# Performance work log

Hardware: AMD Instinct MI355X
Metric: run time of the kernel (lower is better)

The kernel has to match this reference:

```python
import jax, jax.numpy as jnp
import numpy as np

N, E, H, S, F = 50000, 800000, 96, 48, 24


def _mlp(x, W1, b1, W2, b2):
    # equinox MLP depth=1: Linear -> relu -> Linear (identity final activation)
    h = jax.nn.relu(x @ W1.T + b1)
    return h @ W2.T + b2


def _segment_softmax(scores, seg, num_segments):
    mx = jax.ops.segment_max(scores, seg, num_segments=num_segments)
    e = jnp.exp(scores - mx[seg])
    s = jax.ops.segment_sum(e, seg, num_segments=num_segments)
    return e / (s[seg] + 1e-9)


def setup_inputs() -> dict:
    key = jax.random.key(0)
    ks = jax.random.split(key, 32)
    def p(i, shape):
        return jax.random.normal(ks[i], shape, dtype=jnp.float32) * 0.05
    in_attn = 2 * H + 2 * S + F   # 312
    w_attn = 2 * H                # 192
    gin = 3 * H                   # 288
    inp = {
        "x": p(0, (N, H)),
        "x_s": p(1, (N, S)),
        "edge_features": p(2, (E, F)),
        "edge_index": jax.random.randint(ks[3], (2, E), 0, N),
        # fwd attention MLP: in_attn -> w_attn -> 1
        "fwd_W1": p(4, (w_attn, in_attn)), "fwd_b1": p(5, (w_attn,)),
        "fwd_W2": p(6, (1, w_attn)), "fwd_b2": p(7, (1,)),
        # rev gate MLP: in_attn -> w_attn -> 1
        "rev_W1": p(8, (w_attn, in_attn)), "rev_b1": p(9, (w_attn,)),
        "rev_W2": p(10, (1, w_attn)), "rev_b2": p(11, (1,)),
        # reset gate MLP: 3H -> 3H -> H
        "reset_W1": p(12, (gin, gin)), "reset_b1": p(13, (gin,)),
        "reset_W2": p(14, (H, gin)), "reset_b2": p(15, (H,)),
        # update gate MLP: 3H -> 3H -> H
        "update_W1": p(16, (gin, gin)), "update_b1": p(17, (gin,)),
        "update_W2": p(18, (H, gin)), "update_b2": p(19, (H,)),
        # candidate MLP: 3H -> 3H -> H
        "cand_W1": p(20, (gin, gin)), "cand_b1": p(21, (gin,)),
        "cand_W2": p(22, (H, gin)), "cand_b2": p(23, (H,)),
    }
    return inp


def reference(x, x_s, edge_features, edge_index,
              fwd_W1, fwd_b1, fwd_W2, fwd_b2,
              rev_W1, rev_b1, rev_W2, rev_b2,
              reset_W1, reset_b1, reset_W2, reset_b2,
              update_W1, update_b1, update_W2, update_b2,
              cand_W1, cand_b1, cand_W2, cand_b2):
    num_nodes = x.shape[0]
    src, dest = edge_index[0], edge_index[1]

    def compute_messages(s, d, W1, b1, W2, b2, use_softmax):
        feat = jnp.concatenate([x[s], x[d], x_s[s], x_s[d], edge_features], axis=-1)
        raw = _mlp(feat, W1, b1, W2, b2)[:, 0]  # [E]
        if use_softmax:
            raw = jax.nn.leaky_relu(raw) / jnp.sqrt(jnp.asarray(x.shape[-1], dtype=x.dtype))
            w = _segment_softmax(raw, d, num_nodes)
        else:
            w = jax.nn.sigmoid(raw)
        agg = jax.ops.segment_sum(x[s] * w[:, None], d, num_segments=num_nodes)
        return agg, w

    fwd_msgs, fwd_w = compute_messages(src, dest, fwd_W1, fwd_b1, fwd_W2, fwd_b2, True)
    rev_msgs, rev_w = compute_messages(dest, src, rev_W1, rev_b1, rev_W2, rev_b2, False)

    messages = jnp.concatenate([fwd_msgs, rev_msgs], axis=-1)  # [N, 2H]
    gate_input = jnp.concatenate([x, messages], axis=-1)        # [N, 3H]
    r_gate = jax.nn.sigmoid(_mlp(gate_input, reset_W1, reset_b1, reset_W2, reset_b2))
    z_gate = jax.nn.sigmoid(_mlp(gate_input, update_W1, update_b1, update_W2, update_b2))
    cand_input = jnp.concatenate([r_gate * x, messages], axis=-1)
    candidate = jnp.tanh(_mlp(cand_input, cand_W1, cand_b1, cand_W2, cand_b2))
    update = (1 - z_gate) * x + z_gate * candidate
    return (update, fwd_w, rev_w, z_gate, r_gate)
```

## Files before the change

### kernel.cpp

```cpp
#include <hip/hip_runtime.h>
#include <math.h>

typedef unsigned short u16;
typedef unsigned int   u32;

#define HDIM 96
#define SDIM 48
#define FDIM 24
#define KA   312
#define WATT 192
#define KG   288

#define KT_A  10
#define KT_G  9
#define NS    296

#define NFRAG (2 * KT_A * 12 * 64)
#define W1F_Q (KT_G * 18 * 64)
#define W2F_Q (KT_G * 6 * 64)
#define NODEF_Q (3 * (W1F_Q + W2F_Q))

#define PB_EDGE 60
#define PB_W1   41
#define PB_W2   14
#define PB_NODE (3 * (PB_W1 + PB_W2))

typedef __attribute__((ext_vector_type(8))) __bf16 bf16x8;
typedef __attribute__((ext_vector_type(4))) float  f32x4;

__device__ __forceinline__ u16 f2bf(float f) {
  u32 u = __float_as_uint(f);
  u = (u + 0x7FFFu + ((u >> 16) & 1u)) >> 16;
  return (u16)u;
}
__device__ __forceinline__ float bf2f(u16 v) {
  return __uint_as_float((u32)v << 16);
}
__device__ __forceinline__ u32 pack2(float a, float b) {
  return (u32)f2bf(a) | ((u32)f2bf(b) << 16);
}
__device__ __forceinline__ f32x4 mfma_bf16(bf16x8 a, bf16x8 b, f32x4 c) {
  return __builtin_amdgcn_mfma_f32_16x16x32_bf16(a, b, c, 0, 0, 0);
}

__global__ __launch_bounds__(256) void prep_all(
    const float* __restrict__ fW1, const float* __restrict__ rW1,
    uint4* __restrict__ Bfrag,
    const float* __restrict__ W1r, const float* __restrict__ W2r,
    const float* __restrict__ W1u, const float* __restrict__ W2u,
    const float* __restrict__ W1c, const float* __restrict__ W2c,
    uint4* __restrict__ NodeF,
    const float* __restrict__ x, const float* __restrict__ xs,
    u32* __restrict__ xb, u32* __restrict__ xsb, int N)
{
  int b = blockIdx.x;
  const int tid = threadIdx.x;

  if (b < PB_EDGE) {
    const int idx = b * 256 + tid;
    const int lane = idx & 63;
    const int frag = idx >> 6;
    const int nt   = frag % 12;
    const int rest = frag / 12;
    const int kt   = rest % KT_A;
    const int mlp  = rest / KT_A;
    const int q = lane >> 4, c = lane & 15;
    const int n  = nt * 16 + c;
    const int p0 = kt * 16 + q * 4;
    const float* W = mlp ? rW1 : fW1;
    u32 v[4];
#pragma unroll
    for (int w = 0; w < 4; ++w) {
      const int p = p0 + w;
      u32 val = 0u;
      if (p < 156) {
        int src = p;
        if (mlp) {
          if (src < 48)       src += 48;
          else if (src < 96)  src -= 48;
          else if (src < 120) src += 24;
          else if (src < 144) src -= 24;
        }
        const float2 wv = *(const float2*)(W + (size_t)n * KA + 2 * src);
        val = pack2(wv.x, wv.y);
      }
      v[w] = val;
    }
    Bfrag[idx] = make_uint4(v[0], v[1], v[2], v[3]);
    return;
  }
  b -= PB_EDGE;

  if (b < PB_NODE) {
    const int mlp = b / (PB_W1 + PB_W2);
    const int lb  = b % (PB_W1 + PB_W2);
    const float* W;
    uint4* o;
    int NT, idx;
    if (lb < PB_W1) {
      NT = 18; idx = lb * 256 + tid;
      W = (mlp == 0) ? W1r : (mlp == 1) ? W1u : W1c;
      o = NodeF + (size_t)mlp * (W1F_Q + W2F_Q);
    } else {
      NT = 6; idx = (lb - PB_W1) * 256 + tid;
      W = (mlp == 0) ? W2r : (mlp == 1) ? W2u : W2c;
      o = NodeF + (size_t)mlp * (W1F_Q + W2F_Q) + W1F_Q;
    }
    if (idx >= KT_G * NT * 64) return;
    const int lane = idx & 63;
    const int frag = idx >> 6;
    const int nt = frag % NT, kt = frag / NT;
    const int q = lane >> 4, c = lane & 15;
    const int n = nt * 16 + c;
    const int k0 = kt * 32 + q * 8;
    u32 v[4];
#pragma unroll
    for (int w = 0; w < 4; ++w) {
      const float2 wv = *(const float2*)(W + (size_t)n * KG + k0 + 2 * w);
      v[w] = pack2(wv.x, wv.y);
    }
    o[idx] = make_uint4(v[0], v[1], v[2], v[3]);
    return;
  }
  b -= PB_NODE;

  {
    const int i = b * 256 + tid;
    const int nx = N * 48;
    if (i < nx) {
      const float2 v = ((const float2*)x)[i];
      xb[i] = pack2(v.x, v.y);
    } else if (i < nx + N * 24) {
      const float2 v = ((const float2*)xs)[i - nx];
      xsb[i - nx] = pack2(v.x, v.y);
    }
  }
}

__global__ __launch_bounds__(256, 2) void edge_kernel(
    const u32* __restrict__ xb, const u32* __restrict__ xsb,
    const float* __restrict__ ef, const int* __restrict__ ei,
    const u16* __restrict__ Bfrag,
    const float* __restrict__ fb1, const float* __restrict__ fW2,
    const float* __restrict__ fb2,
    const float* __restrict__ rb1, const float* __restrict__ rW2,
    const float* __restrict__ rb2,
    float* __restrict__ pe, float* __restrict__ out_revw, int N, int E)
{
  __shared__ float red[2][4][64];

  const int tid  = threadIdx.x;
  const int wave = tid >> 6, lane = tid & 63;
  const int q = lane >> 4, c = lane & 15;
  const int e0 = blockIdx.x * 64;

  int em[4], sm[4], dm[4];
#pragma unroll
  for (int m = 0; m < 4; ++m) {
    em[m] = min(e0 + m * 16 + c, E - 1);
    int s = ei[em[m]], d = ei[(size_t)E + em[m]];
    sm[m] = min(max(s, 0), N - 1);
    dm[m] = min(max(d, 0), N - 1);
  }

  const bf16x8* __restrict__ Bf = (const bf16x8*)Bfrag;

  f32x4 accF[4][3], accR[4][3];
#pragma unroll
  for (int m = 0; m < 4; ++m)
    for (int t = 0; t < 3; ++t) {
      accF[m][t] = (f32x4){0.f, 0.f, 0.f, 0.f};
      accR[m][t] = (f32x4){0.f, 0.f, 0.f, 0.f};
    }

#pragma unroll
  for (int kt = 0; kt < KT_A; ++kt) {
    const int p0 = kt * 16 + q * 4;
    bf16x8 a[4];
#pragma unroll
    for (int m = 0; m < 4; ++m) {
      uint4 av;
      if (kt < 3) {
        av = *(const uint4*)(xb + (size_t)sm[m] * 48 + p0);
      } else if (kt < 6) {
        av = *(const uint4*)(xb + (size_t)dm[m] * 48 + (p0 - 48));
      } else if (kt == 6) {
        av = *(const uint4*)(xsb + (size_t)sm[m] * 24 + (p0 - 96));
      } else if (kt == 7) {
        const u32* p = (q < 2) ? xsb + (size_t)sm[m] * 24 + (p0 - 96)
                               : xsb + (size_t)dm[m] * 24 + (p0 - 120);
        av = *(const uint4*)p;
      } else if (kt == 8) {
        av = *(const uint4*)(xsb + (size_t)dm[m] * 24 + (p0 - 120));
      } else {
        if (q < 3) {
          const float* efp = ef + (size_t)em[m] * 24 + (p0 - 144) * 2;
          const float4 f0 = *(const float4*)efp;
          const float4 f1 = *(const float4*)(efp + 4);
          av = make_uint4(pack2(f0.x, f0.y), pack2(f0.z, f0.w),
                          pack2(f1.x, f1.y), pack2(f1.z, f1.w));
        } else {
          av = make_uint4(0u, 0u, 0u, 0u);
        }
      }
      a[m] = __builtin_bit_cast(bf16x8, av);
    }
#pragma unroll
    for (int t = 0; t < 3; ++t) {
      const bf16x8 bF = Bf[((kt * 12) + wave * 3 + t) * 64 + lane];
      const bf16x8 bR = Bf[(((KT_A + kt) * 12) + wave * 3 + t) * 64 + lane];
#pragma unroll
      for (int m = 0; m < 4; ++m) {
        accF[m][t] = mfma_bf16(a[m], bF, accF[m][t]);
        accR[m][t] = mfma_bf16(a[m], bR, accR[m][t]);
      }
    }
  }

  float pf[4][4], pr[4][4];
#pragma unroll
  for (int m = 0; m < 4; ++m)
    for (int r = 0; r < 4; ++r) { pf[m][r] = 0.f; pr[m][r] = 0.f; }
#pragma unroll
  for (int t = 0; t < 3; ++t) {
    const int n = (wave * 3 + t) * 16 + c;
    const float fb = fb1[n], fw = fW2[n];
    const float rb = rb1[n], rw = rW2[n];
#pragma unroll
    for (int m = 0; m < 4; ++m)
      for (int r = 0; r < 4; ++r) {
        float hf = accF[m][t][r] + fb;
        hf = hf > 0.f ? hf : 0.f;
        pf[m][r] += hf * fw;
        float hr = accR[m][t][r] + rb;
        hr = hr > 0.f ? hr : 0.f;
        pr[m][r] += hr * rw;
      }
  }
  for (int off = 1; off <= 8; off <<= 1)
#pragma unroll
    for (int m = 0; m < 4; ++m)
      for (int r = 0; r < 4; ++r) {
        pf[m][r] += __shfl_xor(pf[m][r], off, 64);
        pr[m][r] += __shfl_xor(pr[m][r], off, 64);
      }

  if (c == 0) {
#pragma unroll
    for (int m = 0; m < 4; ++m)
      for (int r = 0; r < 4; ++r) {
        red[0][wave][m * 16 + q * 4 + r] = pf[m][r];
        red[1][wave][m * 16 + q * 4 + r] = pr[m][r];
      }
  }
  __syncthreads();

  if (tid < 64 && e0 + tid < E) {
    const int e = e0 + tid;
    float rawf = red[0][0][tid] + red[0][1][tid] + red[0][2][tid] + red[0][3][tid];
    rawf += fb2[0];
    const float lr = rawf > 0.f ? rawf : 0.01f * rawf;
    pe[e] = __expf(lr * 0.10206207261596575f);
    float rawr = red[1][0][tid] + red[1][1][tid] + red[1][2][tid] + red[1][3][tid];
    rawr += rb2[0];
    out_revw[e] = 1.f / (1.f + __expf(-rawr));
  }
}

__global__ __launch_bounds__(256) void k_hist(
    const int* __restrict__ ei, int* __restrict__ deg_d,
    int* __restrict__ deg_s, int N, int E)
{
  const int e = blockIdx.x * 256 + threadIdx.x;
  if (e >= E) return;
  const int s = min(max(ei[e], 0), N - 1);
  const int d = min(max(ei[(size_t)E + e], 0), N - 1);
  atomicAdd(&deg_d[d], 1);
  atomicAdd(&deg_s[s], 1);
}

__global__ __launch_bounds__(256) void k_scan1(
    const int* __restrict__ deg_d, const int* __restrict__ deg_s,
    int* __restrict__ start_d, int* __restrict__ start_s,
    int* __restrict__ bsum_d, int* __restrict__ bsum_s, int N)
{
  __shared__ int sh[256];
  const int t = threadIdx.x, i = blockIdx.x * 256 + t;
  {
    const int v = (i < N) ? deg_d[i] : 0;
    sh[t] = v; __syncthreads();
    for (int off = 1; off < 256; off <<= 1) {
      const int u = (t >= off) ? sh[t - off] : 0;
      __syncthreads();
      sh[t] += u;
      __syncthreads();
    }
    if (i < N) start_d[i] = sh[t] - v;
    if (t == 255) bsum_d[blockIdx.x] = sh[255];
    __syncthreads();
  }
  {
    const int v = (i < N) ? deg_s[i] : 0;
    sh[t] = v; __syncthreads();
    for (int off = 1; off < 256; off <<= 1) {
      const int u = (t >= off) ? sh[t - off] : 0;
      __syncthreads();
      sh[t] += u;
      __syncthreads();
    }
    if (i < N) start_s[i] = sh[t] - v;
    if (t == 255) bsum_s[blockIdx.x] = sh[255];
  }
}

__global__ __launch_bounds__(256) void k_scan3(
    int* __restrict__ start_d, int* __restrict__ start_s,
    const int* __restrict__ bsum_d, const int* __restrict__ bsum_s,
    int* __restrict__ pos_d, int* __restrict__ pos_s, int N)
{
  __shared__ int offs[2];
  const int t = threadIdx.x;
  if (t < 2) {
    const int* bs = t ? bsum_s : bsum_d;
    int r = 0;
    for (int bb = 0; bb < (int)blockIdx.x; ++bb) r += bs[bb];
    offs[t] = r;
  }
  __syncthreads();
  const int i = blockIdx.x * 256 + t;
  if (i >= N) return;
  const int vd = start_d[i] + offs[0]; start_d[i] = vd; pos_d[i] = vd;
  const int vs = start_s[i] + offs[1]; start_s[i] = vs; pos_s[i] = vs;
}

__global__ __launch_bounds__(256) void k_fill(
    const int* __restrict__ ei, int* __restrict__ pos_d,
    int* __restrict__ pos_s, int* __restrict__ eidx_d,
    int* __restrict__ eidx_s, int N, int E)
{
  const int e = blockIdx.x * 256 + threadIdx.x;
  if (e >= E) return;
  const int s = min(max(ei[e], 0), N - 1);
  const int d = min(max(ei[(size_t)E + e], 0), N - 1);
  eidx_d[atomicAdd(&pos_d[d], 1)] = e;
  eidx_s[atomicAdd(&pos_s[s], 1)] = e;
}

__global__ __launch_bounds__(256) void k_agg_all(
    const float* __restrict__ x, const int* __restrict__ ei,
    const float* __restrict__ pe, const float* __restrict__ revw,
    const int* __restrict__ start_d, const int* __restrict__ end_d,
    const int* __restrict__ eidx_d,
    const int* __restrict__ start_s, const int* __restrict__ end_s,
    const int* __restrict__ eidx_s,
    u16* __restrict__ fwdm, u16* __restrict__ revm,
    float* __restrict__ out_fwdw, int N, int E, int ablk)
{
  int b = blockIdx.x;
  const int dir = (b >= ablk) ? 1 : 0;
  if (dir) b -= ablk;
  const int g = threadIdx.x >> 5;
  const int l = threadIdx.x & 31;
  const int n = b * 8 + g;
  if (n >= N) return;

  const int* start = dir ? start_s : start_d;
  const int* endp  = dir ? end_s   : end_d;
  const int* eidx  = dir ? eidx_s  : eidx_d;
  const int beg = start[n], end = endp[n];

  float inv = 1.f;
  if (dir == 0) {
    float sum = 0.f;
    for (int i = beg + l; i < end; i += 32) sum += pe[eidx[i]];
    for (int off = 16; off; off >>= 1) sum += __shfl_xor(sum, off, 32);
    inv = 1.f / (sum + 1e-9f);
    for (int i = beg + l; i < end; i += 32) {
      const int e = eidx[i];
      out_fwdw[e] = pe[e] * inv;
    }
  }

  float a0 = 0.f, a1 = 0.f, a2 = 0.f;
  for (int i = beg; i < end; ++i) {
    const int e = eidx[i];
    const float w = (dir == 0) ? pe[e] * inv : revw[e];
    const int o = (dir == 0) ? min(max(ei[e], 0), N - 1)
                             : min(max(ei[(size_t)E + e], 0), N - 1);
    const float* xr = x + (size_t)o * 96;
    a0 += w * xr[l];
    a1 += w * xr[l + 32];
    a2 += w * xr[l + 64];
  }
  u16* orow = (dir ? revm : fwdm) + (size_t)n * 96;
  orow[l] = f2bf(a0); orow[l + 32] = f2bf(a1); orow[l + 64] = f2bf(a2);
}

__device__ __forceinline__ void node_mlp(
    const u16* __restrict__ Alds, u16* __restrict__ Hlds,
    const bf16x8* __restrict__ W1f, const bf16x8* __restrict__ W2f,
    const float* __restrict__ b1,
    int wave, int lane, int q, int c, int ntc, int ntc2,
    f32x4 (&acc2)[4][2])
{
  f32x4 acc[4][5];
#pragma unroll
  for (int m = 0; m < 4; ++m)
    for (int t = 0; t < 5; ++t) acc[m][t] = (f32x4){0.f, 0.f, 0.f, 0.f};

#pragma unroll
  for (int kt = 0; kt < KT_G; ++kt) {
    bf16x8 a[4];
#pragma unroll
    for (int m = 0; m < 4; ++m)
      a[m] = *(const bf16x8*)&Alds[(m * 16 + c) * NS + kt * 32 + q * 8];
#pragma unroll
    for (int t = 0; t < 5; ++t) {
      if (t < ntc) {
        const int nt = wave + 4 * t;
        const bf16x8 b = W1f[(kt * 18 + nt) * 64 + lane];
#pragma unroll
        for (int m = 0; m < 4; ++m)
          acc[m][t] = mfma_bf16(a[m], b, acc[m][t]);
      }
    }
  }

  __syncthreads();
#pragma unroll
  for (int t = 0; t < 5; ++t) {
    if (t < ntc) {
      const int n = (wave + 4 * t) * 16 + c;
      const float b1f = b1[n];
#pragma unroll
      for (int m = 0; m < 4; ++m)
        for (int r = 0; r < 4; ++r) {
          float h = acc[m][t][r] + b1f;
          h = h > 0.f ? h : 0.f;
          Hlds[(m * 16 + q * 4 + r) * NS + n] = f2bf(h);
        }
    }
  }
  __syncthreads();

#pragma unroll
  for (int m = 0; m < 4; ++m)
    for (int t = 0; t < 2; ++t) acc2[m][t] = (f32x4){0.f, 0.f, 0.f, 0.f};
#pragma unroll
  for (int kt = 0; kt < KT_G; ++kt) {
    bf16x8 a[4];
#pragma unroll
    for (int m = 0; m < 4; ++m)
      a[m] = *(const bf16x8*)&Hlds[(m * 16 + c) * NS + kt * 32 + q * 8];
#pragma unroll
    for (int t = 0; t < 2; ++t) {
      if (t < ntc2) {
        const int nt = wave + 4 * t;
        const bf16x8 b = W2f[(kt * 6 + nt) * 64 + lane];
#pragma unroll
        for (int m = 0; m < 4; ++m)
          acc2[m][t] = mfma_bf16(a[m], b, acc2[m][t]);
      }
    }
  }
}

__global__ __launch_bounds__(256, 2) void node_fused(
    const float* __restrict__ x, const u32* __restrict__ xb,
    const u32* __restrict__ fwdmb, const u32* __restrict__ revmb,
    const uint4* __restrict__ NodeF,
    const float* __restrict__ b1r, const float* __restrict__ b2r,
    const float* __restrict__ b1u, const float* __restrict__ b2u,
    const float* __restrict__ b1c, const float* __restrict__ b2c,
    float* __restrict__ out_r, float* __restrict__ out_z,
    float* __restrict__ out_upd, int N)
{
  __shared__ __align__(16) u16 Alds[64 * NS];
  __shared__ __align__(16) u16 Hlds[64 * NS];

  const int tid = threadIdx.x;
  const int wave = tid >> 6, lane = tid & 63;
  const int q = lane >> 4, c = lane & 15;
  const int n0 = blockIdx.x * 64;
  const int ntc  = (wave < 2) ? 5 : 4;
  const int ntc2 = (wave < 2) ? 2 : 1;

  {
    const int nl = tid >> 2, sub = tid & 3;
    const int node = min(n0 + nl, N - 1);
    const uint4* xr = (const uint4*)(xb    + (size_t)node * 48);
    const uint4* fr = (const uint4*)(fwdmb + (size_t)node * 48);
    const uint4* rr = (const uint4*)(revmb + (size_t)node * 48);
    uint4* Arow = (uint4*)&Alds[nl * NS];
    if (sub == 0) {
      uint4 t0 = xr[0], t1 = xr[1], t2 = xr[2], t3 = xr[3], t4 = xr[4],
            t5 = xr[5], t6 = xr[6], t7 = xr[7], t8 = xr[8];
      Arow[0] = t0; Arow[1] = t1; Arow[2] = t2; Arow[3] = t3; Arow[4] = t4;
      Arow[5] = t5; Arow[6] = t6; Arow[7] = t7; Arow[8] = t8;
    } else if (sub == 1) {
      uint4 t0 = xr[9], t1 = xr[10], t2 = xr[11], t3 = fr[0], t4 = fr[1],
            t5 = fr[2], t6 = fr[3], t7 = fr[4], t8 = fr[5];
      Arow[9] = t0; Arow[10] = t1; Arow[11] = t2; Arow[12] = t3;
      Arow[13] = t4; Arow[14] = t5; Arow[15] = t6; Arow[16] = t7;
      Arow[17] = t8;
    } else if (sub == 2) {
      uint4 t0 = fr[6], t1 = fr[7], t2 = fr[8], t3 = fr[9], t4 = fr[10],
            t5 = fr[11], t6 = rr[0], t7 = rr[1], t8 = rr[2];
      Arow[18] = t0; Arow[19] = t1; Arow[20] = t2; Arow[21] = t3;
      Arow[22] = t4; Arow[23] = t5; Arow[24] = t6; Arow[25] = t7;
      Arow[26] = t8;
    } else {
      uint4 t0 = rr[3], t1 = rr[4], t2 = rr[5], t3 = rr[6], t4 = rr[7],
            t5 = rr[8], t6 = rr[9], t7 = rr[10], t8 = rr[11];
      Arow[27] = t0; Arow[28] = t1; Arow[29] = t2; Arow[30] = t3;
      Arow[31] = t4; Arow[32] = t5; Arow[33] = t6; Arow[34] = t7;
      Arow[35] = t8;
    }
  }
  __syncthreads();

  const bf16x8* W1fr = (const bf16x8*)(NodeF);
  const bf16x8* W2fr = (const bf16x8*)(NodeF + W1F_Q);
  const bf16x8* W1fu = (const bf16x8*)(NodeF + W1F_Q + W2F_Q);
  const bf16x8* W2fu = (const bf16x8*)(NodeF + 2 * W1F_Q + W2F_Q);
  const bf16x8* W1fc = (const bf16x8*)(NodeF + 2 * (W1F_Q + W2F_Q));
  const bf16x8* W2fc = (const bf16x8*)(NodeF + 3 * W1F_Q + 2 * W2F_Q);

  f32x4 acc2[4][2];

  node_mlp(Alds, Hlds, W1fr, W2fr, b1r, wave, lane, q, c, ntc, ntc2, acc2);
  float r_reg[2][4][4];
#pragma unroll
  for (int t = 0; t < 2; ++t) {
    if (t < ntc2) {
      const int n2 = (wave + 4 * t) * 16 + c;
      const float b2f = b2r[n2];
#pragma unroll
      for (int m = 0; m < 4; ++m)
        for (int r = 0; r < 4; ++r) {
          const float v = acc2[m][t][r] + b2f;
          const float rv = 1.f / (1.f + __expf(-v));
          r_reg[t][m][r] = rv;
          const int node = n0 + m * 16 + q * 4 + r;
          if (node < N) out_r[(size_t)node * HDIM + n2] = rv;
        }
    }
  }

  node_mlp(Alds, Hlds, W1fu, W2fu, b1u, wave, lane, q, c, ntc, ntc2, acc2);
  float z_reg[2][4][4];
#pragma unroll
  for (int t = 0; t < 2; ++t) {
    if (t < ntc2) {
      const int n2 = (wave + 4 * t) * 16 + c;
      const float b2f = b2u[n2];
#pragma unroll
      for (int m = 0; m < 4; ++m)
        for (int r = 0; r < 4; ++r) {
          const float v = acc2[m][t][r] + b2f;
          const float zv = 1.f / (1.f + __expf(-v));
          z_reg[t][m][r] = zv;
          const int node = n0 + m * 16 + q * 4 + r;
          if (node < N) out_z[(size_t)node * HDIM + n2] = zv;
        }
    }
  }

#pragma unroll
  for (int t = 0; t < 2; ++t) {
    if (t < ntc2) {
      const int n2 = (wave + 4 * t) * 16 + c;
#pragma unroll
      for (int m = 0; m < 4; ++m)
        for (int r = 0; r < 4; ++r) {
          const int row = m * 16 + q * 4 + r;
          const int idx = row * NS + n2;
          Alds[idx] = f2bf(bf2f(Alds[idx]) * r_reg[t][m][r]);
        }
    }
  }
  __syncthreads();

  node_mlp(Alds, Hlds, W1fc, W2fc, b1c, wave, lane, q, c, ntc, ntc2, acc2);
#pragma unroll
  for (int t = 0; t < 2; ++t) {
    if (t < ntc2) {
      const int n2 = (wave + 4 * t) * 16 + c;
      const float b2f = b2c[n2];
#pragma unroll
      for (int m = 0; m < 4; ++m)
        for (int r = 0; r < 4; ++r) {
          const int node = n0 + m * 16 + q * 4 + r;
          if (node < N) {
            const float v = acc2[m][t][r] + b2f;
            const float ct = tanhf(v);
            const float z = z_reg[t][m][r];
            const float xv = x[(size_t)node * HDIM + n2];
            out_upd[(size_t)node * HDIM + n2] = (1.f - z) * xv + z * ct;
          }
        }
    }
  }
}

__global__ void sentinel_kernel(float* out, int n, float val) {
  const int i = blockIdx.x * 256 + threadIdx.x;
  if (i < n) out[i] = val;
}

extern "C" void kernel_launch(void* const* d_in, const int* in_sizes, int n_in,
                              void* d_out, int out_size, void* d_ws, size_t ws_size,
                              hipStream_t stream) {
  const float* x  = (const float*)d_in[0];
  const float* xs = (const float*)d_in[1];
  const float* ef = (const float*)d_in[2];
  const int*   ei = (const int*)d_in[3];

  const int N = in_sizes[0] / HDIM;
  const int E = in_sizes[3] / 2;

  float* out = (float*)d_out;

  const int NB = (N + 255) / 256;

  const bool sizes_ok =
      n_in == 24 && NB <= 1024 &&
      in_sizes[0] == N * HDIM && in_sizes[1] == N * SDIM &&
      in_sizes[2] == E * FDIM && in_sizes[3] == 2 * E &&
      in_sizes[4] == WATT * KA && in_sizes[5] == WATT &&
      in_sizes[6] == WATT && in_sizes[7] == 1 &&
      in_sizes[12] == KG * KG && in_sizes[13] == KG &&
      in_sizes[14] == HDIM * KG && in_sizes[15] == HDIM &&
      out_size == 3 * N * HDIM + 2 * E;
  if (!sizes_ok) {
    sentinel_kernel<<<(out_size + 255) / 256, 256, 0, stream>>>(out, out_size, 777.0f);
    return;
  }

  const size_t eA = ((size_t)E + 3) & ~(size_t)3;
  const size_t needed =
      (eA + (size_t)NFRAG * 4 + (size_t)NODEF_Q * 4 +
       (size_t)N * 48 + (size_t)N * 24 + 2 * (size_t)N * 48 +
       6 * (size_t)N + 2048 + 2 * (size_t)E) * 4;
  if (ws_size < needed) {
    sentinel_kernel<<<(out_size + 255) / 256, 256, 0, stream>>>(out, out_size, 12345.0f);
    return;
  }
  float* pe    = (float*)d_ws;
  uint4* Bfrag = (uint4*)((u32*)d_ws + eA);
  uint4* NodeF = Bfrag + NFRAG;
  u32*   xbw   = (u32*)(NodeF + NODEF_Q);
  u32*   xsbw  = xbw + (size_t)N * 48;
  u32*   fwdmb = xsbw + (size_t)N * 24;
  u32*   revmb = fwdmb + (size_t)N * 48;
  int* deg_d   = (int*)(revmb + (size_t)N * 48);
  int* deg_s   = deg_d + N;
  int* start_d = deg_s + N;
  int* start_s = start_d + N;
  int* pos_d   = start_s + N;
  int* pos_s   = pos_d + N;
  int* bsum_d  = pos_s + N;
  int* bsum_s  = bsum_d + 1024;
  int* eidx_d  = bsum_s + 1024;
  int* eidx_s  = eidx_d + E;

  float* out_update = out;
  float* out_fwdw   = out + (size_t)N * HDIM;
  float* out_revw   = out_fwdw + E;
  float* out_z      = out_revw + E;
  float* out_r      = out_z + (size_t)N * HDIM;

  (void)hipMemsetAsync(deg_d, 0, 2 * (size_t)N * sizeof(int), stream);

  const int prep_blocks = PB_EDGE + PB_NODE + (N * 72 + 255) / 256;
  prep_all<<<prep_blocks, 256, 0, stream>>>(
      (const float*)d_in[4], (const float*)d_in[8], Bfrag,
      (const float*)d_in[12], (const float*)d_in[14],
      (const float*)d_in[16], (const float*)d_in[18],
      (const float*)d_in[20], (const float*)d_in[22], NodeF,
      x, xs, xbw, xsbw, N);

  const int eblk = (E + 255) / 256;
  k_hist<<<eblk, 256, 0, stream>>>(ei, deg_d, deg_s, N, E);
  k_scan1<<<NB, 256, 0, stream>>>(deg_d, deg_s, start_d, start_s,
                                  bsum_d, bsum_s, N);
  k_scan3<<<NB, 256, 0, stream>>>(start_d, start_s, bsum_d, bsum_s,
                                  pos_d, pos_s, N);
  k_fill<<<eblk, 256, 0, stream>>>(ei, pos_d, pos_s, eidx_d, eidx_s, N, E);

  edge_kernel<<<(E + 63) / 64, 256, 0, stream>>>(
      xbw, xsbw, ef, ei, (const u16*)Bfrag,
      (const float*)d_in[5], (const float*)d_in[6], (const float*)d_in[7],
      (const float*)d_in[9], (const float*)d_in[10], (const float*)d_in[11],
      pe, out_revw, N, E);

  const int ablk = (N + 7) / 8;
  k_agg_all<<<2 * ablk, 256, 0, stream>>>(
      x, ei, pe, out_revw,
      start_d, pos_d, eidx_d, start_s, pos_s, eidx_s,
      (u16*)fwdmb, (u16*)revmb, out_fwdw, N, E, ablk);

  const int nblk = (N + 63) / 64;
  node_fused<<<nblk, 256, 0, stream>>>(
      x, xbw, fwdmb, revmb, NodeF,
      (const float*)d_in[13], (const float*)d_in[15],
      (const float*)d_in[17], (const float*)d_in[19],
      (const float*)d_in[21], (const float*)d_in[23],
      out_r, out_z, out_update, N);
}
```

Baseline: 1.111 ms.

## Split forward and reverse attention MLPs across separate waves in edge kernel

The edge kernel now launches 512 threads (8 waves): the first four waves compute the forward attention MLP and the last four compute the reverse gate MLP, where before each wave computed both. This halves the accumulator registers per wave and raises the launch-bounds occupancy target, aiming to hide gather latency with more resident waves. In exchange, each A-operand gather (node features, edge features) is now loaded twice per block, once per wave group, which adds memory traffic.

```diff
diff --git a/kernel.cpp b/kernel.cpp
--- a/kernel.cpp
+++ b/kernel.cpp
@@ -137,7 +137,7 @@
   }
 }
 
-__global__ __launch_bounds__(256, 2) void edge_kernel(
+__global__ __launch_bounds__(512, 4) void edge_kernel(
     const u32* __restrict__ xb, const u32* __restrict__ xsb,
     const float* __restrict__ ef, const int* __restrict__ ei,
     const u16* __restrict__ Bfrag,
@@ -151,6 +151,8 @@
 
   const int tid  = threadIdx.x;
   const int wave = tid >> 6, lane = tid & 63;
+  const int mlp  = wave >> 2;
+  const int w4   = wave & 3;
   const int q = lane >> 4, c = lane & 15;
   const int e0 = blockIdx.x * 64;
 
@@ -165,13 +167,11 @@
 
   const bf16x8* __restrict__ Bf = (const bf16x8*)Bfrag;
 
-  f32x4 accF[4][3], accR[4][3];
+  f32x4 acc[4][3];
 #pragma unroll
   for (int m = 0; m < 4; ++m)
-    for (int t = 0; t < 3; ++t) {
-      accF[m][t] = (f32x4){0.f, 0.f, 0.f, 0.f};
-      accR[m][t] = (f32x4){0.f, 0.f, 0.f, 0.f};
-    }
+    for (int t = 0; t < 3; ++t)
+      acc[m][t] = (f32x4){0.f, 0.f, 0.f, 0.f};
 
 #pragma unroll
   for (int kt = 0; kt < KT_A; ++kt) {
@@ -207,51 +207,43 @@
     }
 #pragma unroll
     for (int t = 0; t < 3; ++t) {
-      const bf16x8 bF = Bf[((kt * 12) + wave * 3 + t) * 64 + lane];
-      const bf16x8 bR = Bf[(((KT_A + kt) * 12) + wave * 3 + t) * 64 + lane];
-#pragma unroll
-      for (int m = 0; m < 4; ++m) {
-        accF[m][t] = mfma_bf16(a[m], bF, accF[m][t]);
-        accR[m][t] = mfma_bf16(a[m], bR, accR[m][t]);
-      }
-    }
-  }
-
-  float pf[4][4], pr[4][4];
+      const bf16x8 b = Bf[(((mlp * KT_A + kt) * 12) + w4 * 3 + t) * 64 + lane];
+#pragma unroll
+      for (int m = 0; m < 4; ++m)
+        acc[m][t] = mfma_bf16(a[m], b, acc[m][t]);
+    }
+  }
+
+  const float* b1p = mlp ? rb1 : fb1;
+  const float* W2p = mlp ? rW2 : fW2;
+  float p[4][4];
 #pragma unroll
   for (int m = 0; m < 4; ++m)
-    for (int r = 0; r < 4; ++r) { pf[m][r] = 0.f; pr[m][r] = 0.f; }
+    for (int r = 0; r < 4; ++r) p[m][r] = 0.f;
 #pragma unroll
   for (int t = 0; t < 3; ++t) {
-    const int n = (wave * 3 + t) * 16 + c;
-    const float fb = fb1[n], fw = fW2[n];
-    const float rb = rb1[n], rw = rW2[n];
+    const int n = (w4 * 3 + t) * 16 + c;
+    const float b1f = b1p[n];
+    const float w2f = W2p[n];
 #pragma unroll
     for (int m = 0; m < 4; ++m)
       for (int r = 0; r < 4; ++r) {
-        float hf = accF[m][t][r] + fb;
-        hf = hf > 0.f ? hf : 0.f;
-        pf[m][r] += hf * fw;
-        float hr = accR[m][t][r] + rb;
-        hr = hr > 0.f ? hr : 0.f;
-        pr[m][r] += hr * rw;
+        float h = acc[m][t][r] + b1f;
+        h = h > 0.f ? h : 0.f;
+        p[m][r] += h * w2f;
       }
   }
   for (int off = 1; off <= 8; off <<= 1)
 #pragma unroll
     for (int m = 0; m < 4; ++m)
-      for (int r = 0; r < 4; ++r) {
-        pf[m][r] += __shfl_xor(pf[m][r], off, 64);
-        pr[m][r] += __shfl_xor(pr[m][r], off, 64);
-      }
+      for (int r = 0; r < 4; ++r)
+        p[m][r] += __shfl_xor(p[m][r], off, 64);
 
   if (c == 0) {
 #pragma unroll
     for (int m = 0; m < 4; ++m)
-      for (int r = 0; r < 4; ++r) {
-        red[0][wave][m * 16 + q * 4 + r] = pf[m][r];
-        red[1][wave][m * 16 + q * 4 + r] = pr[m][r];
-      }
+      for (int r = 0; r < 4; ++r)
+        red[mlp][w4][m * 16 + q * 4 + r] = p[m][r];
   }
   __syncthreads();
 
@@ -688,7 +680,7 @@
                                   pos_d, pos_s, N);
   k_fill<<<eblk, 256, 0, stream>>>(ei, pos_d, pos_s, eidx_d, eidx_s, N, E);
 
-  edge_kernel<<<(E + 63) / 64, 256, 0, stream>>>(
+  edge_kernel<<<(E + 63) / 64, 512, 0, stream>>>(
       xbw, xsbw, ef, ei, (const u16*)Bfrag,
       (const float*)d_in[5], (const float*)d_in[6], (const float*)d_in[7],
       (const float*)d_in[9], (const float*)d_in[10], (const float*)d_in[11],
```

New measurement: 1.115 ms. About the same (+0.3%).
